# Kernel optimization log

Measured on AMD Instinct MI355X. Metric: run time of the kernel, lower is better.

## Reference

```python
import jax, jax.numpy as jnp
import numpy as np

N = 50000
E = 800000
IN_DIM = 128
EMB_DIM = 64
HID = 128
OUT_DIM = 64
VOCAB = 1000
NUM_GRAPHS = 128


def _gat(x, src, dst, W, a_s, a_d, b, n):
    # PyG GATConv, heads=1: h = x @ W (no bias); alpha_e = leaky_relu(a_s.h_src + a_d.h_dst, 0.2)
    h = x @ W                                  # [n, C]
    as_n = h @ a_s                             # [n]
    ad_n = h @ a_d                             # [n]
    logit = jax.nn.leaky_relu(as_n[src] + ad_n[dst], negative_slope=0.2)  # [E']
    # segment softmax over destination node
    m = jax.ops.segment_max(logit, dst, num_segments=n)
    e = jnp.exp(logit - m[dst])
    s = jax.ops.segment_sum(e, dst, num_segments=n)
    coef = e / s[dst]                          # [E']
    out = jax.ops.segment_sum(h[src] * coef[:, None], dst, num_segments=n)
    return out + b


def setup_inputs() -> dict:
    key = jax.random.key(0)
    ks = jax.random.split(key, 20)
    inp = {
        "x": jax.random.normal(ks[0], (N, IN_DIM), dtype=jnp.float32),
        "node_index": jax.random.randint(ks[1], (N,), 0, VOCAB),
        "edge_index": jax.random.randint(ks[2], (2, E), 0, N),
        "batch": jnp.sort(jax.random.randint(ks[3], (N,), 0, NUM_GRAPHS)),
        "emb": jax.random.normal(ks[4], (VOCAB, EMB_DIM), dtype=jnp.float32) * 0.1,
        "W1": jax.random.normal(ks[5], (IN_DIM + EMB_DIM, HID), dtype=jnp.float32) * 0.05,
        "a1s": jax.random.normal(ks[6], (HID,), dtype=jnp.float32) * 0.1,
        "a1d": jax.random.normal(ks[7], (HID,), dtype=jnp.float32) * 0.1,
        "b1": jnp.zeros((HID,), dtype=jnp.float32),
        "W2": jax.random.normal(ks[8], (HID, HID), dtype=jnp.float32) * 0.05,
        "a2s": jax.random.normal(ks[9], (HID,), dtype=jnp.float32) * 0.1,
        "a2d": jax.random.normal(ks[10], (HID,), dtype=jnp.float32) * 0.1,
        "b2": jnp.zeros((HID,), dtype=jnp.float32),
        "W3": jax.random.normal(ks[11], (HID, HID), dtype=jnp.float32) * 0.05,
        "a3s": jax.random.normal(ks[12], (HID,), dtype=jnp.float32) * 0.1,
        "a3d": jax.random.normal(ks[13], (HID,), dtype=jnp.float32) * 0.1,
        "b3": jnp.zeros((HID,), dtype=jnp.float32),
        "fcW": jax.random.normal(ks[14], (HID, OUT_DIM), dtype=jnp.float32) * 0.05,
        "fcb": jnp.zeros((OUT_DIM,), dtype=jnp.float32),
    }
    return inp


def reference(x, node_index, edge_index, batch, emb, W1, a1s, a1d, b1,
              W2, a2s, a2d, b2, W3, a3s, a3d, b3, fcW, fcb):
    n = x.shape[0]
    # embedding lookup + L2 normalize features, then concat
    ev = emb[node_index]                       # [N, EMB_DIM]
    norms = jnp.linalg.norm(x, axis=1, keepdims=True)
    norms = jnp.where(norms == 0, 1e-8, norms)
    h = jnp.concatenate([x / norms, ev], axis=1)  # [N, IN+EMB]
    # add self loops (PyG GATConv default add_self_loops=True)
    loop = jnp.arange(n)
    src = jnp.concatenate([edge_index[0], loop])
    dst = jnp.concatenate([edge_index[1], loop])
    h = jax.nn.gelu(_gat(h, src, dst, W1, a1s, a1d, b1, n))
    h = jax.nn.gelu(_gat(h, src, dst, W2, a2s, a2d, b2, n))
    h = jax.nn.gelu(_gat(h, src, dst, W3, a3s, a3d, b3, n))
    # global_add_pool over graphs
    g = jax.ops.segment_sum(h, batch, num_segments=NUM_GRAPHS)  # [G, HID]
    out = g @ fcW + fcb
    return jax.nn.leaky_relu(out, negative_slope=0.01)
```

## Files before the change

### kernel.cpp

```cpp
#include <hip/hip_runtime.h>

#define N_NODES 50000
#define N_EDGES 800000
#define IN_DIM 128
#define EMB_DIM 64
#define HID 128
#define OUT_DIM 64
#define NUM_GRAPHS 128
#define E_TOT (N_EDGES + N_NODES)
#define K1 (IN_DIM + EMB_DIM)
#define NB 391
#define EPT 16
#define EPB (256 * EPT)

typedef __attribute__((ext_vector_type(8))) short bf16x8;
typedef __attribute__((ext_vector_type(4))) float f32x4;

__device__ __forceinline__ float gelu_f(float x) {
    float x3 = x * x * x;
    return 0.5f * x * (1.0f + tanhf(0.7978845608028654f * (x + 0.044715f * x3)));
}
__device__ __forceinline__ float lrelu02(float x) { return x > 0.f ? x : 0.2f * x; }
__device__ __forceinline__ float rl_f(float v, int j) {
    return __int_as_float(__builtin_amdgcn_readlane(__float_as_int(v), j));
}
__device__ __forceinline__ unsigned short f2bf(float f) {
    unsigned u = __float_as_uint(f);
    unsigned r = (u + 0x7fffu + ((u >> 16) & 1u)) >> 16;
    return (unsigned short)r;
}
__device__ __forceinline__ unsigned pk2bf(float a, float b) {
    return (unsigned)f2bf(a) | ((unsigned)f2bf(b) << 16);
}

__global__ __launch_bounds__(256) void k_zero(int* __restrict__ bcnt, int* __restrict__ bfill) {
    int t = blockIdx.x * 256 + threadIdx.x;
    if (t < NB) { bcnt[t] = 0; bfill[t] = 0; }
}

__global__ __launch_bounds__(128) void k_prepW3(const float* __restrict__ W1, unsigned short* __restrict__ Wt1,
                                                const float* __restrict__ W2, unsigned short* __restrict__ Wt2,
                                                const float* __restrict__ W3, unsigned short* __restrict__ Wt3) {
    int b = blockIdx.x;
    int c = threadIdx.x;
    if (b < K1) {
        Wt1[(size_t)c * (K1 + 8) + b] = f2bf(W1[(size_t)b * HID + c]);
    } else if (b < K1 + HID) {
        int k = b - K1;
        Wt2[(size_t)c * (HID + 8) + k] = f2bf(W2[(size_t)k * HID + c]);
    } else {
        int k = b - K1 - HID;
        Wt3[(size_t)c * (HID + 8) + k] = f2bf(W3[(size_t)k * HID + c]);
    }
}

__global__ __launch_bounds__(256) void k_prepA(const float* __restrict__ x, const int* __restrict__ nidx,
                                               const float* __restrict__ emb, unsigned* __restrict__ Abu) {
    int lane = threadIdx.x & 63;
    int node = (blockIdx.x * 256 + threadIdx.x) >> 6;
    if (node >= N_NODES) return;
    float2 v = ((const float2*)(x + (size_t)node * IN_DIM))[lane];
    float ss = v.x * v.x + v.y * v.y;
#pragma unroll
    for (int o = 32; o; o >>= 1) ss += __shfl_xor(ss, o);
    float nrm = sqrtf(ss);
    if (nrm == 0.f) nrm = 1e-8f;
    float inv = 1.f / nrm;
    unsigned* row = Abu + (size_t)node * (K1 / 2);
    row[lane] = pk2bf(v.x * inv, v.y * inv);
    int nid = __builtin_amdgcn_readfirstlane(nidx[node]);
    if (lane < 32) {
        float2 e = ((const float2*)(emb + (size_t)nid * EMB_DIM))[lane];
        row[64 + lane] = pk2bf(e.x, e.y);
    }
}

__global__ __launch_bounds__(256) void k_bhist(const int* __restrict__ dst, int* __restrict__ bcnt) {
    __shared__ int h[NB];
    for (int i = threadIdx.x; i < NB; i += 256) h[i] = 0;
    __syncthreads();
    for (int e = blockIdx.x * 256 + threadIdx.x; e < N_EDGES; e += gridDim.x * 256)
        atomicAdd(&h[dst[e] >> 7], 1);
    __syncthreads();
    for (int i = threadIdx.x; i < NB; i += 256)
        if (h[i]) atomicAdd(&bcnt[i], h[i]);
}

__global__ __launch_bounds__(512) void k_bscan(const int* __restrict__ bcnt, int* __restrict__ boff,
                                               int* __restrict__ rowptr) {
    __shared__ int sh[512];
    int t = threadIdx.x;
    int v = (t < NB) ? bcnt[t] : 0;
    sh[t] = v;
    __syncthreads();
    for (int o = 1; o < 512; o <<= 1) {
        int u = (t >= o) ? sh[t - o] : 0;
        __syncthreads();
        sh[t] += u;
        __syncthreads();
    }
    if (t < NB) boff[t] = sh[t] - v;
    if (t == NB - 1) boff[NB] = sh[t];
    if (t == 0) rowptr[N_NODES] = E_TOT;
}

__global__ __launch_bounds__(256) void k_passA(const int* __restrict__ src, const int* __restrict__ dst,
                                               const int* __restrict__ boff, int* __restrict__ bfill,
                                               unsigned* __restrict__ barr) {
    __shared__ int h[NB];
    __shared__ int base[NB];
    for (int i = threadIdx.x; i < NB; i += 256) h[i] = 0;
    __syncthreads();
    int e0 = blockIdx.x * EPB;
    int tag[EPT];
#pragma unroll
    for (int i = 0; i < EPT; i++) {
        int e = e0 + i * 256 + threadIdx.x;
        tag[i] = -1;
        if (e < N_EDGES) {
            int b = dst[e] >> 7;
            int r = atomicAdd(&h[b], 1);
            tag[i] = (b << 12) | r;
        }
    }
    __syncthreads();
    for (int i = threadIdx.x; i < NB; i += 256)
        base[i] = h[i] ? atomicAdd(&bfill[i], h[i]) : 0;
    __syncthreads();
#pragma unroll
    for (int i = 0; i < EPT; i++) {
        if (tag[i] >= 0) {
            int e = e0 + i * 256 + threadIdx.x;
            int b = tag[i] >> 12, r = tag[i] & 0xfff;
            unsigned s = (unsigned)src[e];
            unsigned dl = (unsigned)(dst[e] & 127);
            barr[boff[b] + base[b] + r] = s | (dl << 16);
        }
    }
}

__global__ __launch_bounds__(256) void k_passB(const unsigned* __restrict__ barr, const int* __restrict__ boff,
                                               int* __restrict__ rowptr, int* __restrict__ csr) {
    __shared__ int dcnt[128];
    __shared__ int dsum[128];
    __shared__ int locOff[128];
    int b = blockIdx.x;
    int t = threadIdx.x;
    int n0 = b << 7;
    int cnt = min(128, N_NODES - n0);
    int eb = boff[b], ee = boff[b + 1];
    if (t < 128) dcnt[t] = 0;
    __syncthreads();
    for (int i = eb + t; i < ee; i += 256) atomicAdd(&dcnt[barr[i] >> 16], 1);
    __syncthreads();
    int v = 0;
    if (t < 128) {
        v = (t < cnt) ? dcnt[t] + 1 : 0;
        dsum[t] = v;
    }
    __syncthreads();
    for (int o = 1; o < 128; o <<= 1) {
        int u = (t >= o && t < 128) ? dsum[t - o] : 0;
        __syncthreads();
        if (t < 128) dsum[t] += u;
        __syncthreads();
    }
    int csrBase = eb + n0;
    if (t < 128) {
        locOff[t] = dsum[t] - v;
        dcnt[t] = 0;
    }
    if (t < cnt) {
        int loc = dsum[t] - v;
        rowptr[n0 + t] = csrBase + loc;
        csr[csrBase + loc] = n0 + t;
    }
    __syncthreads();
    for (int i = eb + t; i < ee; i += 256) {
        unsigned vv = barr[i];
        int dl = vv >> 16;
        int s = (int)(vv & 0xffffu);
        int k = atomicAdd(&dcnt[dl], 1);
        csr[csrBase + locOff[dl] + 1 + k] = s;
    }
}

template <int K>
__global__ __launch_bounds__(256) void k_mgemm(const unsigned short* __restrict__ Abf,
                                               const unsigned short* __restrict__ WtP,
                                               const float* __restrict__ a_s, const float* __restrict__ a_d,
                                               unsigned short* __restrict__ Hbf,
                                               float* __restrict__ asn, float* __restrict__ adn) {
    constexpr int KP = K + 8;
    constexpr int NK = K / 32;
    __shared__ __align__(16) unsigned short Wl[128 * KP];
    {
        const uint4* gsrc = (const uint4*)WtP;
        uint4* ldst = (uint4*)Wl;
        const int nchunk = 128 * KP * 2 / 16;
        for (int i = threadIdx.x; i < nchunk; i += 256) ldst[i] = gsrc[i];
    }
    int lane = threadIdx.x & 63;
    int wv = threadIdx.x >> 6;
    int rowbase = blockIdx.x * 64 + wv * 16;
    if (rowbase >= N_NODES) { __syncthreads(); return; }
    int l15 = lane & 15, quad = lane >> 4;

    const unsigned short* Abase = Abf + (size_t)(rowbase + l15) * K + quad * 8;
    bf16x8 afr[NK];
#pragma unroll
    for (int i = 0; i < NK; i++) afr[i] = *(const bf16x8*)(Abase + i * 32);

    __syncthreads();

    f32x4 acc[8];
#pragma unroll
    for (int t = 0; t < 8; t++) acc[t] = (f32x4){0.f, 0.f, 0.f, 0.f};
#pragma unroll
    for (int i = 0; i < NK; i++) {
#pragma unroll
        for (int t = 0; t < 8; t++) {
            bf16x8 bf = *(const bf16x8*)(&Wl[(t * 16 + l15) * KP + i * 32 + quad * 8]);
            acc[t] = __builtin_amdgcn_mfma_f32_16x16x32_bf16(afr[i], bf, acc[t], 0, 0, 0);
        }
    }
    float asc[8], adc[8];
#pragma unroll
    for (int t = 0; t < 8; t++) { asc[t] = a_s[t * 16 + l15]; adc[t] = a_d[t * 16 + l15]; }
#pragma unroll
    for (int r = 0; r < 4; r++) {
        int row = rowbase + quad * 4 + r;
        float ps = 0.f, pd = 0.f;
#pragma unroll
        for (int t = 0; t < 8; t++) {
            float v = acc[t][r];
            Hbf[(size_t)row * HID + t * 16 + l15] = f2bf(v);
            ps = fmaf(v, asc[t], ps);
            pd = fmaf(v, adc[t], pd);
        }
#pragma unroll
        for (int o = 1; o < 16; o <<= 1) {
            ps += __shfl_xor(ps, o);
            pd += __shfl_xor(pd, o);
        }
        if (l15 == 0) { asn[row] = ps; adn[row] = pd; }
    }
}

template <bool OUT32>
__global__ __launch_bounds__(256) void k_aggr(const int* __restrict__ rowptr, const int* __restrict__ csr,
                                              const float* __restrict__ asn, const float* __restrict__ adn,
                                              const unsigned short* __restrict__ hbf,
                                              const float* __restrict__ bias, void* __restrict__ outp) {
    __shared__ float sh_e[4][64];
    __shared__ int sh_s[4][64];
    int lane = threadIdx.x & 63;
    int w = threadIdx.x >> 6;
    int node = blockIdx.x * 4 + w;
    if (node >= N_NODES) return;
    int st = rowptr[node], en = rowptr[node + 1];
    int deg = en - st;
    float ad = adn[node];
    const unsigned* hu = (const unsigned*)hbf;
    float2 acc = make_float2(0.f, 0.f);

    if (deg <= 64) {
        int s = 0;
        float l = -1e30f;
        if (lane < deg) {
            s = csr[st + lane];
            l = lrelu02(asn[s] + ad);
        }
        float m = l;
#pragma unroll
        for (int o = 32; o; o >>= 1) m = fmaxf(m, __shfl_xor(m, o));
        float e = (lane < deg) ? __expf(l - m) : 0.f;
        float ssum = e;
#pragma unroll
        for (int o = 32; o; o >>= 1) ssum += __shfl_xor(ssum, o);
        float coef = e / ssum;
        int j = 0;
        for (; j + 8 <= deg; j += 8) {
            int si[8];
            float ci[8];
            unsigned vi[8];
#pragma unroll
            for (int q = 0; q < 8; q++) {
                si[q] = __builtin_amdgcn_readlane(s, j + q);
                ci[q] = rl_f(coef, j + q);
            }
#pragma unroll
            for (int q = 0; q < 8; q++) vi[q] = hu[(size_t)si[q] * 64 + lane];
#pragma unroll
            for (int q = 0; q < 8; q++) {
                acc.x = fmaf(ci[q], __int_as_float(vi[q] << 16), acc.x);
                acc.y = fmaf(ci[q], __int_as_float(vi[q] & 0xffff0000u), acc.y);
            }
        }
        for (; j + 4 <= deg; j += 4) {
            int s0 = __builtin_amdgcn_readlane(s, j);
            int s1 = __builtin_amdgcn_readlane(s, j + 1);
            int s2 = __builtin_amdgcn_readlane(s, j + 2);
            int s3 = __builtin_amdgcn_readlane(s, j + 3);
            float c0 = rl_f(coef, j), c1 = rl_f(coef, j + 1);
            float c2 = rl_f(coef, j + 2), c3 = rl_f(coef, j + 3);
            unsigned v0 = hu[(size_t)s0 * 64 + lane];
            unsigned v1 = hu[(size_t)s1 * 64 + lane];
            unsigned v2 = hu[(size_t)s2 * 64 + lane];
            unsigned v3 = hu[(size_t)s3 * 64 + lane];
            acc.x = fmaf(c0, __int_as_float(v0 << 16), acc.x);
            acc.y = fmaf(c0, __int_as_float(v0 & 0xffff0000u), acc.y);
            acc.x = fmaf(c1, __int_as_float(v1 << 16), acc.x);
            acc.y = fmaf(c1, __int_as_float(v1 & 0xffff0000u), acc.y);
            acc.x = fmaf(c2, __int_as_float(v2 << 16), acc.x);
            acc.y = fmaf(c2, __int_as_float(v2 & 0xffff0000u), acc.y);
            acc.x = fmaf(c3, __int_as_float(v3 << 16), acc.x);
            acc.y = fmaf(c3, __int_as_float(v3 & 0xffff0000u), acc.y);
        }
        for (; j < deg; j++) {
            int s0 = __builtin_amdgcn_readlane(s, j);
            float c0 = rl_f(coef, j);
            unsigned v0 = hu[(size_t)s0 * 64 + lane];
            acc.x = fmaf(c0, __int_as_float(v0 << 16), acc.x);
            acc.y = fmaf(c0, __int_as_float(v0 & 0xffff0000u), acc.y);
        }
    } else {
        float m = -1e30f;
        for (int i = st + lane; i < en; i += 64) {
            float l = lrelu02(asn[csr[i]] + ad);
            m = fmaxf(m, l);
        }
#pragma unroll
        for (int o = 32; o; o >>= 1) m = fmaxf(m, __shfl_xor(m, o));
        float ssum = 0.f;
        for (int i = st + lane; i < en; i += 64) {
            float l = lrelu02(asn[csr[i]] + ad);
            ssum += __expf(l - m);
        }
#pragma unroll
        for (int o = 32; o; o >>= 1) ssum += __shfl_xor(ssum, o);
        float inv = 1.f / ssum;
        for (int base = st; base < en; base += 64) {
            int cnt = min(64, en - base);
            if (lane < cnt) {
                int sx = csr[base + lane];
                float l = lrelu02(asn[sx] + ad);
                sh_e[w][lane] = __expf(l - m) * inv;
                sh_s[w][lane] = sx;
            }
            for (int j = 0; j < cnt; j++) {
                float c = sh_e[w][j];
                int sx = sh_s[w][j];
                unsigned v0 = hu[(size_t)sx * 64 + lane];
                acc.x = fmaf(c, __int_as_float(v0 << 16), acc.x);
                acc.y = fmaf(c, __int_as_float(v0 & 0xffff0000u), acc.y);
            }
        }
    }
    float2 b = ((const float2*)bias)[lane];
    float rx = gelu_f(acc.x + b.x);
    float ry = gelu_f(acc.y + b.y);
    if constexpr (OUT32) {
        ((float2*)outp)[(size_t)node * 64 + lane] = make_float2(rx, ry);
    } else {
        ((unsigned*)outp)[(size_t)node * 64 + lane] = pk2bf(rx, ry);
    }
}

__global__ __launch_bounds__(256) void k_poolfc(const float* __restrict__ h, const int* __restrict__ batch,
                                                const float* __restrict__ fcW, const float* __restrict__ fcb,
                                                float* __restrict__ out) {
    __shared__ float gv[HID];
    __shared__ float tmp[256];
    int g = blockIdx.x;
    int st, en;
    {
        int lo = 0, hi = N_NODES;
        while (lo < hi) { int mid = (lo + hi) >> 1; if (batch[mid] < g) lo = mid + 1; else hi = mid; }
        st = lo;
        lo = st; hi = N_NODES;
        while (lo < hi) { int mid = (lo + hi) >> 1; if (batch[mid] < g + 1) lo = mid + 1; else hi = mid; }
        en = lo;
    }
    int c = threadIdx.x & 127;
    int half = threadIdx.x >> 7;
    float acc = 0.f;
#pragma unroll 4
    for (int n = st + half; n < en; n += 2) acc += h[(size_t)n * HID + c];
    tmp[threadIdx.x] = acc;
    __syncthreads();
    if (threadIdx.x < HID) gv[threadIdx.x] = tmp[threadIdx.x] + tmp[threadIdx.x + 128];
    __syncthreads();
    if (threadIdx.x < OUT_DIM) {
        float a = fcb[threadIdx.x];
#pragma unroll 4
        for (int k = 0; k < HID; k++) a = fmaf(gv[k], fcW[k * OUT_DIM + threadIdx.x], a);
        out[g * OUT_DIM + threadIdx.x] = a > 0.f ? a : 0.01f * a;
    }
}

extern "C" void kernel_launch(void* const* d_in, const int* in_sizes, int n_in,
                              void* d_out, int out_size, void* d_ws, size_t ws_size,
                              hipStream_t stream) {
    const float* x    = (const float*)d_in[0];
    const int* nidx   = (const int*)d_in[1];
    const int* ei     = (const int*)d_in[2];
    const int* batch  = (const int*)d_in[3];
    const float* emb  = (const float*)d_in[4];
    const float* W1   = (const float*)d_in[5];
    const float* a1s  = (const float*)d_in[6];
    const float* a1d  = (const float*)d_in[7];
    const float* b1   = (const float*)d_in[8];
    const float* W2   = (const float*)d_in[9];
    const float* a2s  = (const float*)d_in[10];
    const float* a2d  = (const float*)d_in[11];
    const float* b2   = (const float*)d_in[12];
    const float* W3   = (const float*)d_in[13];
    const float* a3s  = (const float*)d_in[14];
    const float* a3d  = (const float*)d_in[15];
    const float* b3   = (const float*)d_in[16];
    const float* fcW  = (const float*)d_in[17];
    const float* fcb  = (const float*)d_in[18];
    float* out = (float*)d_out;
    const int* srcA = ei;
    const int* dstA = ei + N_EDGES;

    char* w = (char*)d_ws;
    auto alloc = [&](size_t bytes) -> char* {
        char* p = w;
        w += (bytes + 511) & ~(size_t)511;
        return p;
    };
    char* region0 = alloc((size_t)N_NODES * HID * 4);
    unsigned* Abu = (unsigned*)region0;
    float* h3f    = (float*)region0;
    unsigned short* hLin = (unsigned short*)alloc((size_t)N_NODES * HID * 2);
    unsigned short* hAct = (unsigned short*)alloc((size_t)N_NODES * HID * 2);
    float* asn   = (float*)alloc((size_t)N_NODES * 4);
    float* adn   = (float*)alloc((size_t)N_NODES * 4);
    int* rowptr  = (int*)alloc((size_t)(N_NODES + 1) * 4);
    int* bcnt    = (int*)alloc((size_t)NB * 4);
    int* boff    = (int*)alloc((size_t)(NB + 1) * 4);
    int* bfill   = (int*)alloc((size_t)NB * 4);
    unsigned* barr = (unsigned*)alloc((size_t)N_EDGES * 4);
    int* csr     = (int*)alloc((size_t)E_TOT * 4);
    unsigned short* Wt1 = (unsigned short*)alloc((size_t)HID * (K1 + 8) * 2);
    unsigned short* Wt2 = (unsigned short*)alloc((size_t)HID * (HID + 8) * 2);
    unsigned short* Wt3 = (unsigned short*)alloc((size_t)HID * (HID + 8) * 2);

    k_zero<<<(NB + 255) / 256, 256, 0, stream>>>(bcnt, bfill);
    k_prepW3<<<K1 + 2 * HID, 128, 0, stream>>>(W1, Wt1, W2, Wt2, W3, Wt3);
    k_prepA<<<(N_NODES + 3) / 4, 256, 0, stream>>>(x, nidx, emb, Abu);

    k_bhist<<<512, 256, 0, stream>>>(dstA, bcnt);
    k_bscan<<<1, 512, 0, stream>>>(bcnt, boff, rowptr);
    k_passA<<<(N_EDGES + EPB - 1) / EPB, 256, 0, stream>>>(srcA, dstA, boff, bfill, barr);
    k_passB<<<NB, 256, 0, stream>>>(barr, boff, rowptr, csr);

    int gemmBlocks = (N_NODES + 63) / 64;
    int aggrBlocks = (N_NODES + 3) / 4;

    k_mgemm<K1><<<gemmBlocks, 256, 0, stream>>>((const unsigned short*)Abu, Wt1, a1s, a1d, hLin, asn, adn);
    k_aggr<false><<<aggrBlocks, 256, 0, stream>>>(rowptr, csr, asn, adn, hLin, b1, hAct);
    k_mgemm<HID><<<gemmBlocks, 256, 0, stream>>>(hAct, Wt2, a2s, a2d, hLin, asn, adn);
    k_aggr<false><<<aggrBlocks, 256, 0, stream>>>(rowptr, csr, asn, adn, hLin, b2, hAct);
    k_mgemm<HID><<<gemmBlocks, 256, 0, stream>>>(hAct, Wt3, a3s, a3d, hLin, asn, adn);
    k_aggr<true><<<aggrBlocks, 256, 0, stream>>>(rowptr, csr, asn, adn, hLin, b3, h3f);

    k_poolfc<<<NUM_GRAPHS, 256, 0, stream>>>(h3f, batch, fcW, fcb, out);
}
```

Before: 331.6 us.

## Gather two edges per wave with 8-byte loads and fuse setup kernels

The aggregation kernel for low-degree nodes now splits the wave into two halves. Each half handles alternate edges and loads 8 bytes per lane (four bf16 features), and the halves are combined with a cross-half shuffle before bias, GELU and the store. This doubles the number of independent gathers in flight and widens each load, which targets the latency of the gather-bound aggregation. Separately, the zeroing kernel is folded into the weight-prep kernel and the edge histogram is merged into the prepA launch, cutting two launches. The cost is extra shuffles and half the lanes sitting idle during the final store.

Result: slower. 339.1 us (+2.2%).

```diff
diff --git a/kernel.cpp b/kernel.cpp
--- a/kernel.cpp
+++ b/kernel.cpp
@@ -12,6 +12,8 @@
 #define NB 391
 #define EPT 16
 #define EPB (256 * EPT)
+#define PREPA_BLOCKS 12500
+#define BHIST_BLOCKS 512
 
 typedef __attribute__((ext_vector_type(8))) short bf16x8;
 typedef __attribute__((ext_vector_type(4))) float f32x4;
@@ -33,16 +35,16 @@
     return (unsigned)f2bf(a) | ((unsigned)f2bf(b) << 16);
 }
 
-__global__ __launch_bounds__(256) void k_zero(int* __restrict__ bcnt, int* __restrict__ bfill) {
-    int t = blockIdx.x * 256 + threadIdx.x;
-    if (t < NB) { bcnt[t] = 0; bfill[t] = 0; }
-}
-
 __global__ __launch_bounds__(128) void k_prepW3(const float* __restrict__ W1, unsigned short* __restrict__ Wt1,
                                                 const float* __restrict__ W2, unsigned short* __restrict__ Wt2,
-                                                const float* __restrict__ W3, unsigned short* __restrict__ Wt3) {
+                                                const float* __restrict__ W3, unsigned short* __restrict__ Wt3,
+                                                int* __restrict__ bcnt, int* __restrict__ bfill) {
     int b = blockIdx.x;
     int c = threadIdx.x;
+    if (b == K1 + 2 * HID) {
+        for (int i = c; i < NB; i += 128) { bcnt[i] = 0; bfill[i] = 0; }
+        return;
+    }
     if (b < K1) {
         Wt1[(size_t)c * (K1 + 8) + b] = f2bf(W1[(size_t)b * HID + c]);
     } else if (b < K1 + HID) {
@@ -54,8 +56,21 @@
     }
 }
 
-__global__ __launch_bounds__(256) void k_prepA(const float* __restrict__ x, const int* __restrict__ nidx,
-                                               const float* __restrict__ emb, unsigned* __restrict__ Abu) {
+__global__ __launch_bounds__(256) void k_prepA_bhist(const float* __restrict__ x, const int* __restrict__ nidx,
+                                                     const float* __restrict__ emb, unsigned* __restrict__ Abu,
+                                                     const int* __restrict__ dst, int* __restrict__ bcnt) {
+    __shared__ int h[NB];
+    if (blockIdx.x >= PREPA_BLOCKS) {
+        int nb = blockIdx.x - PREPA_BLOCKS;
+        for (int i = threadIdx.x; i < NB; i += 256) h[i] = 0;
+        __syncthreads();
+        for (int e = nb * 256 + threadIdx.x; e < N_EDGES; e += BHIST_BLOCKS * 256)
+            atomicAdd(&h[dst[e] >> 7], 1);
+        __syncthreads();
+        for (int i = threadIdx.x; i < NB; i += 256)
+            if (h[i]) atomicAdd(&bcnt[i], h[i]);
+        return;
+    }
     int lane = threadIdx.x & 63;
     int node = (blockIdx.x * 256 + threadIdx.x) >> 6;
     if (node >= N_NODES) return;
@@ -73,17 +88,6 @@
         float2 e = ((const float2*)(emb + (size_t)nid * EMB_DIM))[lane];
         row[64 + lane] = pk2bf(e.x, e.y);
     }
-}
-
-__global__ __launch_bounds__(256) void k_bhist(const int* __restrict__ dst, int* __restrict__ bcnt) {
-    __shared__ int h[NB];
-    for (int i = threadIdx.x; i < NB; i += 256) h[i] = 0;
-    __syncthreads();
-    for (int e = blockIdx.x * 256 + threadIdx.x; e < N_EDGES; e += gridDim.x * 256)
-        atomicAdd(&h[dst[e] >> 7], 1);
-    __syncthreads();
-    for (int i = threadIdx.x; i < NB; i += 256)
-        if (h[i]) atomicAdd(&bcnt[i], h[i]);
 }
 
 __global__ __launch_bounds__(512) void k_bscan(const int* __restrict__ bcnt, int* __restrict__ boff,
@@ -261,8 +265,6 @@
     int st = rowptr[node], en = rowptr[node + 1];
     int deg = en - st;
     float ad = adn[node];
-    const unsigned* hu = (const unsigned*)hbf;
-    float2 acc = make_float2(0.f, 0.f);
 
     if (deg <= 64) {
         int s = 0;
@@ -279,52 +281,86 @@
 #pragma unroll
         for (int o = 32; o; o >>= 1) ssum += __shfl_xor(ssum, o);
         float coef = e / ssum;
+
+        const uint2* hu2 = (const uint2*)hbf;
+        int half = lane >> 5, li = lane & 31;
+        float4 acc = make_float4(0.f, 0.f, 0.f, 0.f);
         int j = 0;
+        for (; j + 16 <= deg; j += 16) {
+            int sx[8];
+            float cf[8];
+            uint2 vv[8];
+#pragma unroll
+            for (int q = 0; q < 8; q++) {
+                int ii = j + 2 * q + half;
+                sx[q] = __shfl(s, ii);
+                cf[q] = __shfl(coef, ii);
+            }
+#pragma unroll
+            for (int q = 0; q < 8; q++) vv[q] = hu2[(size_t)sx[q] * 32 + li];
+#pragma unroll
+            for (int q = 0; q < 8; q++) {
+                acc.x = fmaf(cf[q], __int_as_float(vv[q].x << 16), acc.x);
+                acc.y = fmaf(cf[q], __int_as_float(vv[q].x & 0xffff0000u), acc.y);
+                acc.z = fmaf(cf[q], __int_as_float(vv[q].y << 16), acc.z);
+                acc.w = fmaf(cf[q], __int_as_float(vv[q].y & 0xffff0000u), acc.w);
+            }
+        }
         for (; j + 8 <= deg; j += 8) {
-            int si[8];
-            float ci[8];
-            unsigned vi[8];
-#pragma unroll
-            for (int q = 0; q < 8; q++) {
-                si[q] = __builtin_amdgcn_readlane(s, j + q);
-                ci[q] = rl_f(coef, j + q);
-            }
-#pragma unroll
-            for (int q = 0; q < 8; q++) vi[q] = hu[(size_t)si[q] * 64 + lane];
-#pragma unroll
-            for (int q = 0; q < 8; q++) {
-                acc.x = fmaf(ci[q], __int_as_float(vi[q] << 16), acc.x);
-                acc.y = fmaf(ci[q], __int_as_float(vi[q] & 0xffff0000u), acc.y);
-            }
-        }
-        for (; j + 4 <= deg; j += 4) {
-            int s0 = __builtin_amdgcn_readlane(s, j);
-            int s1 = __builtin_amdgcn_readlane(s, j + 1);
-            int s2 = __builtin_amdgcn_readlane(s, j + 2);
-            int s3 = __builtin_amdgcn_readlane(s, j + 3);
-            float c0 = rl_f(coef, j), c1 = rl_f(coef, j + 1);
-            float c2 = rl_f(coef, j + 2), c3 = rl_f(coef, j + 3);
-            unsigned v0 = hu[(size_t)s0 * 64 + lane];
-            unsigned v1 = hu[(size_t)s1 * 64 + lane];
-            unsigned v2 = hu[(size_t)s2 * 64 + lane];
-            unsigned v3 = hu[(size_t)s3 * 64 + lane];
-            acc.x = fmaf(c0, __int_as_float(v0 << 16), acc.x);
-            acc.y = fmaf(c0, __int_as_float(v0 & 0xffff0000u), acc.y);
-            acc.x = fmaf(c1, __int_as_float(v1 << 16), acc.x);
-            acc.y = fmaf(c1, __int_as_float(v1 & 0xffff0000u), acc.y);
-            acc.x = fmaf(c2, __int_as_float(v2 << 16), acc.x);
-            acc.y = fmaf(c2, __int_as_float(v2 & 0xffff0000u), acc.y);
-            acc.x = fmaf(c3, __int_as_float(v3 << 16), acc.x);
-            acc.y = fmaf(c3, __int_as_float(v3 & 0xffff0000u), acc.y);
-        }
-        for (; j < deg; j++) {
-            int s0 = __builtin_amdgcn_readlane(s, j);
-            float c0 = rl_f(coef, j);
-            unsigned v0 = hu[(size_t)s0 * 64 + lane];
-            acc.x = fmaf(c0, __int_as_float(v0 << 16), acc.x);
-            acc.y = fmaf(c0, __int_as_float(v0 & 0xffff0000u), acc.y);
+            int sx[4];
+            float cf[4];
+            uint2 vv[4];
+#pragma unroll
+            for (int q = 0; q < 4; q++) {
+                int ii = j + 2 * q + half;
+                sx[q] = __shfl(s, ii);
+                cf[q] = __shfl(coef, ii);
+            }
+#pragma unroll
+            for (int q = 0; q < 4; q++) vv[q] = hu2[(size_t)sx[q] * 32 + li];
+#pragma unroll
+            for (int q = 0; q < 4; q++) {
+                acc.x = fmaf(cf[q], __int_as_float(vv[q].x << 16), acc.x);
+                acc.y = fmaf(cf[q], __int_as_float(vv[q].x & 0xffff0000u), acc.y);
+                acc.z = fmaf(cf[q], __int_as_float(vv[q].y << 16), acc.z);
+                acc.w = fmaf(cf[q], __int_as_float(vv[q].y & 0xffff0000u), acc.w);
+            }
+        }
+        for (; j < deg; j += 2) {
+            int ii = j + half;
+            int ok = ii < deg;
+            int ic = ok ? ii : j;
+            int sx = __shfl(s, ic);
+            float cf = __shfl(coef, ic);
+            if (!ok) cf = 0.f;
+            uint2 v = hu2[(size_t)sx * 32 + li];
+            acc.x = fmaf(cf, __int_as_float(v.x << 16), acc.x);
+            acc.y = fmaf(cf, __int_as_float(v.x & 0xffff0000u), acc.y);
+            acc.z = fmaf(cf, __int_as_float(v.y << 16), acc.z);
+            acc.w = fmaf(cf, __int_as_float(v.y & 0xffff0000u), acc.w);
+        }
+        acc.x += __shfl_xor(acc.x, 32);
+        acc.y += __shfl_xor(acc.y, 32);
+        acc.z += __shfl_xor(acc.z, 32);
+        acc.w += __shfl_xor(acc.w, 32);
+        float4 bb = ((const float4*)bias)[li];
+        float r0 = gelu_f(acc.x + bb.x);
+        float r1 = gelu_f(acc.y + bb.y);
+        float r2 = gelu_f(acc.z + bb.z);
+        float r3 = gelu_f(acc.w + bb.w);
+        if (half == 0) {
+            if constexpr (OUT32) {
+                ((float4*)outp)[(size_t)node * 32 + li] = make_float4(r0, r1, r2, r3);
+            } else {
+                uint2 o;
+                o.x = pk2bf(r0, r1);
+                o.y = pk2bf(r2, r3);
+                ((uint2*)outp)[(size_t)node * 32 + li] = o;
+            }
         }
     } else {
+        const unsigned* hu = (const unsigned*)hbf;
+        float2 acc = make_float2(0.f, 0.f);
         float m = -1e30f;
         for (int i = st + lane; i < en; i += 64) {
             float l = lrelu02(asn[csr[i]] + ad);
@@ -356,14 +392,14 @@
                 acc.y = fmaf(c, __int_as_float(v0 & 0xffff0000u), acc.y);
             }
         }
-    }
-    float2 b = ((const float2*)bias)[lane];
-    float rx = gelu_f(acc.x + b.x);
-    float ry = gelu_f(acc.y + b.y);
-    if constexpr (OUT32) {
-        ((float2*)outp)[(size_t)node * 64 + lane] = make_float2(rx, ry);
-    } else {
-        ((unsigned*)outp)[(size_t)node * 64 + lane] = pk2bf(rx, ry);
+        float2 b = ((const float2*)bias)[lane];
+        float rx = gelu_f(acc.x + b.x);
+        float ry = gelu_f(acc.y + b.y);
+        if constexpr (OUT32) {
+            ((float2*)outp)[(size_t)node * 64 + lane] = make_float2(rx, ry);
+        } else {
+            ((unsigned*)outp)[(size_t)node * 64 + lane] = pk2bf(rx, ry);
+        }
     }
 }
 
@@ -448,11 +484,9 @@
     unsigned short* Wt2 = (unsigned short*)alloc((size_t)HID * (HID + 8) * 2);
     unsigned short* Wt3 = (unsigned short*)alloc((size_t)HID * (HID + 8) * 2);
 
-    k_zero<<<(NB + 255) / 256, 256, 0, stream>>>(bcnt, bfill);
-    k_prepW3<<<K1 + 2 * HID, 128, 0, stream>>>(W1, Wt1, W2, Wt2, W3, Wt3);
-    k_prepA<<<(N_NODES + 3) / 4, 256, 0, stream>>>(x, nidx, emb, Abu);
-
-    k_bhist<<<512, 256, 0, stream>>>(dstA, bcnt);
+    k_prepW3<<<K1 + 2 * HID + 1, 128, 0, stream>>>(W1, Wt1, W2, Wt2, W3, Wt3, bcnt, bfill);
+    k_prepA_bhist<<<PREPA_BLOCKS + BHIST_BLOCKS, 256, 0, stream>>>(x, nidx, emb, Abu, dstA, bcnt);
+
     k_bscan<<<1, 512, 0, stream>>>(bcnt, boff, rowptr);
     k_passA<<<(N_EDGES + EPB - 1) / EPB, 256, 0, stream>>>(srcA, dstA, boff, bfill, barr);
     k_passB<<<NB, 256, 0, stream>>>(barr, boff, rowptr, csr);
```
